# Optimization experiments

Measured on AMD Instinct MI355X. Metric: run time of the kernel, lower is better.

Reference implementation:

```python
import jax, jax.numpy as jnp
import numpy as np

B, S, D, H = 4, 2048, 1024, 16
HD = D // H  # head dim = 64

def setup_inputs() -> dict:
    key = jax.random.key(0)
    ks = jax.random.split(key, 11)
    s = 1.0 / np.sqrt(D)
    return {
        "q": jax.random.normal(ks[0], (B, S, D), jnp.float32),
        "k": jax.random.normal(ks[1], (B, S, D), jnp.float32),
        "v": jax.random.normal(ks[2], (B, S, D), jnp.float32),
        "Wq": jax.random.normal(ks[3], (D, D), jnp.float32) * s,
        "bq": jnp.zeros((D,), jnp.float32),
        "Wk": jax.random.normal(ks[4], (D, D), jnp.float32) * s,
        "bk": jnp.zeros((D,), jnp.float32),
        "Wv": jax.random.normal(ks[5], (D, D), jnp.float32) * s,
        "bv": jnp.zeros((D,), jnp.float32),
        "Wo": jax.random.normal(ks[6], (D, D), jnp.float32) * s,
        "bo": jnp.zeros((D,), jnp.float32),
    }

def reference(q, k, v, Wq, bq, Wk, bk, Wv, bv, Wo, bo):
    b, n, _ = q.shape
    # QKV projections, split heads -> [b, s, h, hd]
    qh = (q @ Wq + bq).reshape(b, n, H, HD)
    kh = (k @ Wk + bk).reshape(b, k.shape[1], H, HD)
    vh = (v @ Wv + bv).reshape(b, v.shape[1], H, HD)
    scale = 1.0 / np.sqrt(HD)
    scores = jnp.einsum('blhe,bshe->bhls', qh, kh)  # [b,h,l,s]
    attn = jax.nn.softmax(scale * scores, axis=-1)  # dropout is identity in eval
    out = jnp.einsum('bhls,bshd->blhd', attn, vh)   # [b,l,h,hd]
    out = out.reshape(b, n, H * HD)
    return out @ Wo + bo
```

## Files before the change

### kernel.cpp

```cpp
#include <hip/hip_runtime.h>
#include <cstdint>

#define DEV __device__ __forceinline__

typedef __attribute__((ext_vector_type(8))) __bf16 bf16x8;
typedef __attribute__((ext_vector_type(2))) unsigned u32x2;
typedef __attribute__((ext_vector_type(4))) float f32x4;

DEV unsigned short f2b(float f) {
  unsigned u = __builtin_bit_cast(unsigned, f);
  u += 0x7fffu + ((u >> 16) & 1u);
  return (unsigned short)(u >> 16);
}

DEV unsigned pkrn(float f0, float f1) {
  unsigned a0 = __builtin_bit_cast(unsigned, f0) + 0x8000u;
  unsigned a1 = __builtin_bit_cast(unsigned, f1) + 0x8000u;
#if __has_builtin(__builtin_amdgcn_perm)
  return __builtin_amdgcn_perm(a1, a0, 0x07060302u);
#else
  return (a0 >> 16) | (a1 & 0xffff0000u);
#endif
}

DEV float exp2_fast(float x) {
#if __has_builtin(__builtin_amdgcn_exp2f)
  return __builtin_amdgcn_exp2f(x);
#else
  return __expf(x * 0.6931471805599453f);
#endif
}

DEV void gload_lds16(const unsigned short* g, unsigned short* l) {
  __builtin_amdgcn_global_load_lds(
      (const __attribute__((address_space(1))) void*)g,
      (__attribute__((address_space(3))) void*)l, 16, 0, 0);
}

__global__ __launch_bounds__(256) void cvt3_kernel(const float* __restrict__ q,
                                                   const float* __restrict__ k,
                                                   const float* __restrict__ v,
                                                   unsigned short* __restrict__ dst) {
  int z = blockIdx.y;
  const float* src = (z == 0) ? q : (z == 1) ? k : v;
  unsigned short* d = dst + (size_t)z * 8192 * 1024;
  int i = blockIdx.x * 256 + threadIdx.x;
  const float4* s4 = (const float4*)src;
  float4 a = s4[2 * i], b = s4[2 * i + 1];
  uint4 o;
  o.x = (unsigned)f2b(a.x) | ((unsigned)f2b(a.y) << 16);
  o.y = (unsigned)f2b(a.z) | ((unsigned)f2b(a.w) << 16);
  o.z = (unsigned)f2b(b.x) | ((unsigned)f2b(b.y) << 16);
  o.w = (unsigned)f2b(b.z) | ((unsigned)f2b(b.w) << 16);
  ((uint4*)d)[i] = o;
}

__global__ __launch_bounds__(256) void wtr4_kernel(const float* __restrict__ W0,
                                                   const float* __restrict__ W1,
                                                   const float* __restrict__ W2,
                                                   const float* __restrict__ W3,
                                                   unsigned short* __restrict__ WtBase) {
  int z = blockIdx.z;
  const float* W = (z == 0) ? W0 : (z == 1) ? W1 : (z == 2) ? W2 : W3;
  unsigned short* Wt = WtBase + (size_t)z * 1024 * 1024;
  __shared__ float t[64][65];
  int n0 = blockIdx.x * 64, k0 = blockIdx.y * 64;
  int tx = threadIdx.x & 63, ty = threadIdx.x >> 6;
  for (int i = ty; i < 64; i += 4)
    t[i][tx] = W[(size_t)(k0 + i) * 1024 + n0 + tx];
  __syncthreads();
  for (int i = ty; i < 64; i += 4)
    Wt[(size_t)(n0 + i) * 1024 + k0 + tx] = f2b(t[tx][i]);
}

struct GemmAcc {
  f32x4 acc[4][4];
};

DEV void gemm_core(const unsigned short* __restrict__ A,
                   const unsigned short* __restrict__ Bt,
                   unsigned short* Al, unsigned short* Bl,
                   int m0, int n0, int K, GemmAcc& R) {
  int tid = threadIdx.x, wv = tid >> 6, ln = tid & 63;
  int wr = wv >> 1, wc = wv & 1;
  for (int i = 0; i < 4; i++)
    for (int j = 0; j < 4; j++) R.acc[i][j] = (f32x4)0.f;
  int lr = ln >> 3, lc = (ln & 7) * 8;
  for (int kt = 0; kt < K; kt += 64) {
    __syncthreads();
    for (int o = 0; o < 4; ++o) {
      int op = wv * 4 + o;
      int row = op * 8 + lr;
      gload_lds16(A + (size_t)(m0 + row) * K + kt + lc, &Al[op * 512]);
    }
    for (int o = 0; o < 4; ++o) {
      int op = wv * 4 + o;
      int row = op * 8 + lr;
      gload_lds16(Bt + (size_t)(n0 + row) * K + kt + lc, &Bl[op * 512]);
    }
    __syncthreads();
    for (int kk = 0; kk < 2; ++kk) {
      bf16x8 af[4], bfr[4];
      int ko = kk * 32 + (ln >> 4) * 8;
      for (int i = 0; i < 4; ++i)
        af[i] = *(const bf16x8*)&Al[(wr * 64 + i * 16 + (ln & 15)) * 64 + ko];
      for (int j = 0; j < 4; ++j)
        bfr[j] = *(const bf16x8*)&Bl[(wc * 64 + j * 16 + (ln & 15)) * 64 + ko];
      for (int i = 0; i < 4; ++i)
        for (int j = 0; j < 4; ++j)
          R.acc[i][j] = __builtin_amdgcn_mfma_f32_16x16x32_bf16(af[i], bfr[j], R.acc[i][j], 0, 0, 0);
    }
  }
}

__global__ __launch_bounds__(256) void gemm_qkv(const unsigned short* __restrict__ Xbase,
                                                const unsigned short* __restrict__ Wbase,
                                                const float* __restrict__ bq,
                                                const float* __restrict__ bk,
                                                const float* __restrict__ bv,
                                                unsigned short* __restrict__ Obase,
                                                float qscale) {
  __shared__ unsigned short Al[128 * 64];
  __shared__ unsigned short Bl[128 * 64];
  int z = blockIdx.z;
  const size_t NX = (size_t)8192 * 1024, NW = (size_t)1024 * 1024;
  const unsigned short* A = Xbase + (size_t)z * NX;
  const unsigned short* Bt = Wbase + (size_t)z * NW;
  const float* bias = (z == 0) ? bq : (z == 1) ? bk : bv;
  unsigned short* outp = Obase + (size_t)z * NX;
  int m0 = blockIdx.y * 128, n0 = blockIdx.x * 128;
  GemmAcc R;
  gemm_core(A, Bt, Al, Bl, m0, n0, 1024, R);
  int ln = threadIdx.x & 63, wv = threadIdx.x >> 6;
  int wr = wv >> 1, wc = wv & 1;
  int g = ln >> 4, c = ln & 15;
  if (z < 2) {
    float oscale = (z == 0) ? qscale : 1.0f;
    for (int j = 0; j < 4; ++j) {
      int gn = n0 + wc * 64 + j * 16 + c;
      float bs = bias[gn];
      int h_ = gn >> 6, hd = gn & 63;
      for (int i = 0; i < 4; ++i) {
        int gm0 = m0 + wr * 64 + i * 16 + g * 4;
        for (int r = 0; r < 4; ++r) {
          float vv = (R.acc[i][j][r] + bs) * oscale;
          int gm = gm0 + r;
          int b_ = gm >> 11, s_ = gm & 2047;
          outp[(((size_t)(b_ * 16 + h_) * 2048 + s_) << 6) + hd] = f2b(vv);
        }
      }
    }
  } else {
    int mb = m0 + wr * 64;
    int b_ = mb >> 11, st = (mb & 2047) >> 6;
    for (int j = 0; j < 4; ++j) {
      int gn = n0 + wc * 64 + j * 16 + c;
      float bs = bias[gn];
      int h_ = gn >> 6, hd = gn & 63;
      unsigned short* vrow = outp + (((size_t)((b_ * 16 + h_) * 32 + st) * 64 + hd) << 6);
      for (int r = 0; r < 4; ++r) {
        u32x2 w;
        w.x = pkrn(R.acc[0][j][r] + bs, R.acc[1][j][r] + bs);
        w.y = pkrn(R.acc[2][j][r] + bs, R.acc[3][j][r] + bs);
        *(u32x2*)&vrow[(g * 4 + r) * 4] = w;
      }
    }
  }
}

__global__ __launch_bounds__(256) void gemm_out(const unsigned short* __restrict__ A,
                                                const unsigned short* __restrict__ Bt,
                                                const float* __restrict__ bias,
                                                float* __restrict__ outp) {
  __shared__ unsigned short Al[128 * 64];
  __shared__ unsigned short Bl[128 * 64];
  int m0 = blockIdx.y * 128, n0 = blockIdx.x * 128;
  GemmAcc R;
  gemm_core(A, Bt, Al, Bl, m0, n0, 1024, R);
  int ln = threadIdx.x & 63, wv = threadIdx.x >> 6;
  int wr = wv >> 1, wc = wv & 1;
  int g = ln >> 4, c = ln & 15;
  for (int j = 0; j < 4; ++j) {
    int gn = n0 + wc * 64 + j * 16 + c;
    float bs = bias[gn];
    for (int i = 0; i < 4; ++i) {
      int gm0 = m0 + wr * 64 + i * 16 + g * 4;
      for (int r = 0; r < 4; ++r)
        outp[(size_t)(gm0 + r) * 1024 + gn] = R.acc[i][j][r] + bs;
    }
  }
}

__global__ __launch_bounds__(256) void attn_kernel(const unsigned short* __restrict__ Qh,
                                                   const unsigned short* __restrict__ Kh,
                                                   const unsigned short* __restrict__ VtG,
                                                   unsigned short* __restrict__ AttnOut) {
  __shared__ unsigned short Kl[64 * 64];
  __shared__ unsigned short Vl[64 * 64];
  __shared__ unsigned short Pl[4 * 32 * 72];
  int tid = threadIdx.x, wv = tid >> 6, ln = tid & 63;
  int qt = blockIdx.x, bh = blockIdx.y;
  const unsigned short* Qb = Qh + (size_t)bh * 2048 * 64;
  const unsigned short* Kb = Kh + (size_t)bh * 2048 * 64;
  const unsigned short* Vb = VtG + (size_t)bh * 2048 * 64;
  int q0 = qt * 128 + wv * 32;
  int g = ln >> 4, c = ln & 15;
  int lr = ln >> 3, lb = ln & 7;
  bf16x8 aq[2][2];
  for (int mi = 0; mi < 2; ++mi)
    for (int kk = 0; kk < 2; ++kk)
      aq[mi][kk] = *(const bf16x8*)(Qb + (size_t)(q0 + mi * 16 + c) * 64 + kk * 32 + g * 8);
  f32x4 o[2][4], lrun[2];
  for (int mi = 0; mi < 2; ++mi) {
    lrun[mi] = (f32x4)0.f;
    for (int j = 0; j < 4; ++j) o[mi][j] = (f32x4)0.f;
  }
  unsigned short* pw = &Pl[wv * 32 * 72];
  for (int kt = 0; kt < 2048; kt += 64) {
    __syncthreads();
    for (int ot = 0; ot < 2; ++ot) {
      int rb = wv * 16 + ot * 8;
      gload_lds16(Kb + (size_t)(kt + rb + lr) * 64 + (lb ^ lr) * 8, &Kl[rb * 64]);
    }
    const unsigned short* vtb = Vb + (size_t)(kt >> 6) * 4096;
    for (int ot = 0; ot < 2; ++ot) {
      int rb = wv * 16 + ot * 8;
      gload_lds16(vtb + (size_t)(rb + lr) * 64 + (lb ^ lr) * 8, &Vl[rb * 64]);
    }
    __syncthreads();
    f32x4 s[2][4];
    for (int mi = 0; mi < 2; ++mi)
      for (int j = 0; j < 4; ++j) s[mi][j] = (f32x4)0.f;
    for (int kk = 0; kk < 2; ++kk) {
      bf16x8 bk[4];
      for (int j = 0; j < 4; ++j)
        bk[j] = *(const bf16x8*)&Kl[(j * 16 + c) * 64 + ((kk * 4 + g) ^ (c & 7)) * 8];
      for (int mi = 0; mi < 2; ++mi)
        for (int j = 0; j < 4; ++j)
          s[mi][j] = __builtin_amdgcn_mfma_f32_16x16x32_bf16(aq[mi][kk], bk[j], s[mi][j], 0, 0, 0);
    }
    for (int mi = 0; mi < 2; ++mi)
      for (int j = 0; j < 4; ++j)
        for (int r = 0; r < 4; ++r) {
          float p = exp2_fast(s[mi][j][r]);
          s[mi][j][r] = p;
          lrun[mi][r] += p;
        }
    for (int mi = 0; mi < 2; ++mi)
      for (int r = 0; r < 4; ++r) {
        u32x2 w;
        w.x = pkrn(s[mi][0][r], s[mi][1][r]);
        w.y = pkrn(s[mi][2][r], s[mi][3][r]);
        *(u32x2*)&pw[(mi * 16 + g * 4 + r) * 72 + c * 4] = w;
      }
    __threadfence_block();
    for (int kk = 0; kk < 2; ++kk) {
      int ko = kk * 32 + g * 8;
      bf16x8 ap[2], bv[4];
      for (int mi = 0; mi < 2; ++mi) ap[mi] = *(const bf16x8*)&pw[(mi * 16 + c) * 72 + ko];
      for (int j = 0; j < 4; ++j)
        bv[j] = *(const bf16x8*)&Vl[(j * 16 + c) * 64 + ((kk * 4 + g) ^ (c & 7)) * 8];
      for (int mi = 0; mi < 2; ++mi)
        for (int j = 0; j < 4; ++j)
          o[mi][j] = __builtin_amdgcn_mfma_f32_16x16x32_bf16(ap[mi], bv[j], o[mi][j], 0, 0, 0);
    }
  }
  int b_ = bh >> 4, h_ = bh & 15;
  for (int mi = 0; mi < 2; ++mi) {
    float linv[4];
    for (int r = 0; r < 4; ++r) {
      float l = lrun[mi][r];
      for (int d = 1; d < 16; d <<= 1) l += __shfl_xor(l, d);
      linv[r] = 1.f / l;
    }
    for (int j = 0; j < 4; ++j)
      for (int r = 0; r < 4; ++r) {
        int row = q0 + mi * 16 + g * 4 + r;
        int col = h_ * 64 + j * 16 + c;
        float val = o[mi][j][r] * linv[r];
        AttnOut[((size_t)b_ * 2048 + row) * 1024 + col] = f2b(val);
      }
  }
}

extern "C" void kernel_launch(void* const* d_in, const int* in_sizes, int n_in,
                              void* d_out, int out_size, void* d_ws, size_t ws_size,
                              hipStream_t stream) {
  const float* q  = (const float*)d_in[0];
  const float* k  = (const float*)d_in[1];
  const float* v  = (const float*)d_in[2];
  const float* Wq = (const float*)d_in[3];
  const float* bq = (const float*)d_in[4];
  const float* Wk = (const float*)d_in[5];
  const float* bk = (const float*)d_in[6];
  const float* Wv = (const float*)d_in[7];
  const float* bv = (const float*)d_in[8];
  const float* Wo = (const float*)d_in[9];
  const float* bo = (const float*)d_in[10];
  float* out = (float*)d_out;

  unsigned short* ws = (unsigned short*)d_ws;
  const size_t NX = (size_t)8192 * 1024;
  const size_t NW = (size_t)1024 * 1024;
  unsigned short* X   = ws;
  unsigned short* Wt  = X + 3 * NX;
  unsigned short* QKV = Wt + 4 * NW;
  unsigned short* Ao  = X;

  const float qscale = 0.125f * 1.4426950408889634f;

  cvt3_kernel<<<dim3(4096, 3), 256, 0, stream>>>(q, k, v, X);
  wtr4_kernel<<<dim3(16, 16, 4), 256, 0, stream>>>(Wq, Wk, Wv, Wo, Wt);
  gemm_qkv<<<dim3(8, 64, 3), 256, 0, stream>>>(X, Wt, bq, bk, bv, QKV, qscale);
  attn_kernel<<<dim3(16, 64), 256, 0, stream>>>(QKV, QKV + NX, QKV + 2 * NX, Ao);
  gemm_out<<<dim3(8, 64), 256, 0, stream>>>(Ao, Wt + 3 * NW, bo, out);
}
```

Measured before the change: 373.7 us.

## Double-buffer LDS tiles in GEMM and attention loops to overlap loads

Both the shared GEMM core and the attention kernel now keep two LDS buffers for their operand tiles. The first tile is loaded before the loop, and each iteration issues the async global-to-LDS loads for the next tile before computing on the current one. This leaves one barrier per iteration instead of two, so memory latency can hide behind MFMA work. The cost is twice the LDS for those tiles (64 KB per GEMM block), which may lower how many blocks fit per CU.

```diff
diff --git a/kernel.cpp b/kernel.cpp
--- a/kernel.cpp
+++ b/kernel.cpp
@@ -86,26 +86,31 @@
   for (int i = 0; i < 4; i++)
     for (int j = 0; j < 4; j++) R.acc[i][j] = (f32x4)0.f;
   int lr = ln >> 3, lc = (ln & 7) * 8;
-  for (int kt = 0; kt < K; kt += 64) {
+  int nk = K >> 6;
+  for (int o = 0; o < 4; ++o) {
+    int op = wv * 4 + o, row = op * 8 + lr;
+    gload_lds16(A + (size_t)(m0 + row) * K + lc, &Al[op * 512]);
+    gload_lds16(Bt + (size_t)(n0 + row) * K + lc, &Bl[op * 512]);
+  }
+  for (int it = 0; it < nk; ++it) {
     __syncthreads();
-    for (int o = 0; o < 4; ++o) {
-      int op = wv * 4 + o;
-      int row = op * 8 + lr;
-      gload_lds16(A + (size_t)(m0 + row) * K + kt + lc, &Al[op * 512]);
-    }
-    for (int o = 0; o < 4; ++o) {
-      int op = wv * 4 + o;
-      int row = op * 8 + lr;
-      gload_lds16(Bt + (size_t)(n0 + row) * K + kt + lc, &Bl[op * 512]);
-    }
-    __syncthreads();
+    int cur = (it & 1) * 8192;
+    if (it + 1 < nk) {
+      int nxt = ((it + 1) & 1) * 8192;
+      int kt = (it + 1) << 6;
+      for (int o = 0; o < 4; ++o) {
+        int op = wv * 4 + o, row = op * 8 + lr;
+        gload_lds16(A + (size_t)(m0 + row) * K + kt + lc, &Al[nxt + op * 512]);
+        gload_lds16(Bt + (size_t)(n0 + row) * K + kt + lc, &Bl[nxt + op * 512]);
+      }
+    }
     for (int kk = 0; kk < 2; ++kk) {
       bf16x8 af[4], bfr[4];
       int ko = kk * 32 + (ln >> 4) * 8;
       for (int i = 0; i < 4; ++i)
-        af[i] = *(const bf16x8*)&Al[(wr * 64 + i * 16 + (ln & 15)) * 64 + ko];
+        af[i] = *(const bf16x8*)&Al[cur + (wr * 64 + i * 16 + (ln & 15)) * 64 + ko];
       for (int j = 0; j < 4; ++j)
-        bfr[j] = *(const bf16x8*)&Bl[(wc * 64 + j * 16 + (ln & 15)) * 64 + ko];
+        bfr[j] = *(const bf16x8*)&Bl[cur + (wc * 64 + j * 16 + (ln & 15)) * 64 + ko];
       for (int i = 0; i < 4; ++i)
         for (int j = 0; j < 4; ++j)
           R.acc[i][j] = __builtin_amdgcn_mfma_f32_16x16x32_bf16(af[i], bfr[j], R.acc[i][j], 0, 0, 0);
@@ -120,8 +125,8 @@
                                                 const float* __restrict__ bv,
                                                 unsigned short* __restrict__ Obase,
                                                 float qscale) {
-  __shared__ unsigned short Al[128 * 64];
-  __shared__ unsigned short Bl[128 * 64];
+  __shared__ unsigned short Al[2 * 128 * 64];
+  __shared__ unsigned short Bl[2 * 128 * 64];
   int z = blockIdx.z;
   const size_t NX = (size_t)8192 * 1024, NW = (size_t)1024 * 1024;
   const unsigned short* A = Xbase + (size_t)z * NX;
@@ -172,8 +177,8 @@
                                                 const unsigned short* __restrict__ Bt,
                                                 const float* __restrict__ bias,
                                                 float* __restrict__ outp) {
-  __shared__ unsigned short Al[128 * 64];
-  __shared__ unsigned short Bl[128 * 64];
+  __shared__ unsigned short Al[2 * 128 * 64];
+  __shared__ unsigned short Bl[2 * 128 * 64];
   int m0 = blockIdx.y * 128, n0 = blockIdx.x * 128;
   GemmAcc R;
   gemm_core(A, Bt, Al, Bl, m0, n0, 1024, R);
@@ -195,8 +200,8 @@
                                                    const unsigned short* __restrict__ Kh,
                                                    const unsigned short* __restrict__ VtG,
                                                    unsigned short* __restrict__ AttnOut) {
-  __shared__ unsigned short Kl[64 * 64];
-  __shared__ unsigned short Vl[64 * 64];
+  __shared__ unsigned short Kl[2 * 64 * 64];
+  __shared__ unsigned short Vl[2 * 64 * 64];
   __shared__ unsigned short Pl[4 * 32 * 72];
   int tid = threadIdx.x, wv = tid >> 6, ln = tid & 63;
   int qt = blockIdx.x, bh = blockIdx.y;
@@ -206,6 +211,7 @@
   int q0 = qt * 128 + wv * 32;
   int g = ln >> 4, c = ln & 15;
   int lr = ln >> 3, lb = ln & 7;
+  int swz = (lb ^ lr) * 8;
   bf16x8 aq[2][2];
   for (int mi = 0; mi < 2; ++mi)
     for (int kk = 0; kk < 2; ++kk)
@@ -216,25 +222,31 @@
     for (int j = 0; j < 4; ++j) o[mi][j] = (f32x4)0.f;
   }
   unsigned short* pw = &Pl[wv * 32 * 72];
-  for (int kt = 0; kt < 2048; kt += 64) {
+  for (int ot = 0; ot < 2; ++ot) {
+    int rb = wv * 16 + ot * 8;
+    gload_lds16(Kb + (size_t)(rb + lr) * 64 + swz, &Kl[rb * 64]);
+    gload_lds16(Vb + (size_t)(rb + lr) * 64 + swz, &Vl[rb * 64]);
+  }
+  for (int t = 0; t < 32; ++t) {
     __syncthreads();
-    for (int ot = 0; ot < 2; ++ot) {
-      int rb = wv * 16 + ot * 8;
-      gload_lds16(Kb + (size_t)(kt + rb + lr) * 64 + (lb ^ lr) * 8, &Kl[rb * 64]);
-    }
-    const unsigned short* vtb = Vb + (size_t)(kt >> 6) * 4096;
-    for (int ot = 0; ot < 2; ++ot) {
-      int rb = wv * 16 + ot * 8;
-      gload_lds16(vtb + (size_t)(rb + lr) * 64 + (lb ^ lr) * 8, &Vl[rb * 64]);
-    }
-    __syncthreads();
+    int cur = (t & 1) * 4096;
+    if (t + 1 < 32) {
+      int nxt = ((t + 1) & 1) * 4096;
+      const unsigned short* kb = Kb + (size_t)(t + 1) * 4096;
+      const unsigned short* vb = Vb + (size_t)(t + 1) * 4096;
+      for (int ot = 0; ot < 2; ++ot) {
+        int rb = wv * 16 + ot * 8;
+        gload_lds16(kb + (size_t)(rb + lr) * 64 + swz, &Kl[nxt + rb * 64]);
+        gload_lds16(vb + (size_t)(rb + lr) * 64 + swz, &Vl[nxt + rb * 64]);
+      }
+    }
     f32x4 s[2][4];
     for (int mi = 0; mi < 2; ++mi)
       for (int j = 0; j < 4; ++j) s[mi][j] = (f32x4)0.f;
     for (int kk = 0; kk < 2; ++kk) {
       bf16x8 bk[4];
       for (int j = 0; j < 4; ++j)
-        bk[j] = *(const bf16x8*)&Kl[(j * 16 + c) * 64 + ((kk * 4 + g) ^ (c & 7)) * 8];
+        bk[j] = *(const bf16x8*)&Kl[cur + (j * 16 + c) * 64 + ((kk * 4 + g) ^ (c & 7)) * 8];
       for (int mi = 0; mi < 2; ++mi)
         for (int j = 0; j < 4; ++j)
           s[mi][j] = __builtin_amdgcn_mfma_f32_16x16x32_bf16(aq[mi][kk], bk[j], s[mi][j], 0, 0, 0);
@@ -259,7 +271,7 @@
       bf16x8 ap[2], bv[4];
       for (int mi = 0; mi < 2; ++mi) ap[mi] = *(const bf16x8*)&pw[(mi * 16 + c) * 72 + ko];
       for (int j = 0; j < 4; ++j)
-        bv[j] = *(const bf16x8*)&Vl[(j * 16 + c) * 64 + ((kk * 4 + g) ^ (c & 7)) * 8];
+        bv[j] = *(const bf16x8*)&Vl[cur + (j * 16 + c) * 64 + ((kk * 4 + g) ^ (c & 7)) * 8];
       for (int mi = 0; mi < 2; ++mi)
         for (int j = 0; j < 4; ++j)
           o[mi][j] = __builtin_amdgcn_mfma_f32_16x16x32_bf16(ap[mi], bv[j], o[mi][j], 0, 0, 0);
```

Result: slower. 384.0 us (+2.8%).

## Double-buffer K/V tiles in attention, switch P and V to fp16, sum rows via MFMA

Applied to the files above, without the earlier changes.

The attention loop now double-buffers K and V in LDS, prefetching the next tile with global_load_lds while the current one is computed, and needs only one barrier per iteration instead of two. Softmax probabilities and V are packed as fp16 with cvt_pkrtz and multiplied with f16 MFMA. Row sums are taken by an extra MFMA against a ones vector, replacing the scalar accumulation and the cross-lane shuffle reduction. The GEMM epilogues also precompute store base addresses. Using fp16 for V and P changes precision and range, and relies on the Q/K projection code producing V in fp16.

```diff
diff --git a/kernel.cpp b/kernel.cpp
--- a/kernel.cpp
+++ b/kernel.cpp
@@ -4,6 +4,8 @@
 #define DEV __device__ __forceinline__
 
 typedef __attribute__((ext_vector_type(8))) __bf16 bf16x8;
+typedef __attribute__((ext_vector_type(8))) _Float16 f16x8;
+typedef __attribute__((ext_vector_type(2))) __fp16 fp16x2;
 typedef __attribute__((ext_vector_type(2))) unsigned u32x2;
 typedef __attribute__((ext_vector_type(4))) float f32x4;
 
@@ -13,14 +15,9 @@
   return (unsigned short)(u >> 16);
 }
 
-DEV unsigned pkrn(float f0, float f1) {
-  unsigned a0 = __builtin_bit_cast(unsigned, f0) + 0x8000u;
-  unsigned a1 = __builtin_bit_cast(unsigned, f1) + 0x8000u;
-#if __has_builtin(__builtin_amdgcn_perm)
-  return __builtin_amdgcn_perm(a1, a0, 0x07060302u);
-#else
-  return (a0 >> 16) | (a1 & 0xffff0000u);
-#endif
+DEV unsigned pkhf(float a, float b) {
+  fp16x2 h = __builtin_amdgcn_cvt_pkrtz(a, b);
+  return __builtin_bit_cast(unsigned, h);
 }
 
 DEV float exp2_fast(float x) {
@@ -134,25 +131,21 @@
   int ln = threadIdx.x & 63, wv = threadIdx.x >> 6;
   int wr = wv >> 1, wc = wv & 1;
   int g = ln >> 4, c = ln & 15;
+  int mb = m0 + wr * 64;
+  int b_ = mb >> 11, sb = mb & 2047;
   if (z < 2) {
     float oscale = (z == 0) ? qscale : 1.0f;
     for (int j = 0; j < 4; ++j) {
       int gn = n0 + wc * 64 + j * 16 + c;
       float bs = bias[gn];
       int h_ = gn >> 6, hd = gn & 63;
-      for (int i = 0; i < 4; ++i) {
-        int gm0 = m0 + wr * 64 + i * 16 + g * 4;
-        for (int r = 0; r < 4; ++r) {
-          float vv = (R.acc[i][j][r] + bs) * oscale;
-          int gm = gm0 + r;
-          int b_ = gm >> 11, s_ = gm & 2047;
-          outp[(((size_t)(b_ * 16 + h_) * 2048 + s_) << 6) + hd] = f2b(vv);
-        }
-      }
+      unsigned short* base = outp + (((size_t)(b_ * 16 + h_) * 2048 + sb + g * 4) << 6) + hd;
+      for (int i = 0; i < 4; ++i)
+        for (int r = 0; r < 4; ++r)
+          base[i * 1024 + r * 64] = f2b((R.acc[i][j][r] + bs) * oscale);
     }
   } else {
-    int mb = m0 + wr * 64;
-    int b_ = mb >> 11, st = (mb & 2047) >> 6;
+    int st = sb >> 6;
     for (int j = 0; j < 4; ++j) {
       int gn = n0 + wc * 64 + j * 16 + c;
       float bs = bias[gn];
@@ -160,8 +153,8 @@
       unsigned short* vrow = outp + (((size_t)((b_ * 16 + h_) * 32 + st) * 64 + hd) << 6);
       for (int r = 0; r < 4; ++r) {
         u32x2 w;
-        w.x = pkrn(R.acc[0][j][r] + bs, R.acc[1][j][r] + bs);
-        w.y = pkrn(R.acc[2][j][r] + bs, R.acc[3][j][r] + bs);
+        w.x = pkhf(R.acc[0][j][r] + bs, R.acc[1][j][r] + bs);
+        w.y = pkhf(R.acc[2][j][r] + bs, R.acc[3][j][r] + bs);
         *(u32x2*)&vrow[(g * 4 + r) * 4] = w;
       }
     }
@@ -183,11 +176,10 @@
   for (int j = 0; j < 4; ++j) {
     int gn = n0 + wc * 64 + j * 16 + c;
     float bs = bias[gn];
-    for (int i = 0; i < 4; ++i) {
-      int gm0 = m0 + wr * 64 + i * 16 + g * 4;
+    float* base = outp + (size_t)(m0 + wr * 64 + g * 4) * 1024 + gn;
+    for (int i = 0; i < 4; ++i)
       for (int r = 0; r < 4; ++r)
-        outp[(size_t)(gm0 + r) * 1024 + gn] = R.acc[i][j][r] + bs;
-    }
+        base[(i * 16 + r) * 1024] = R.acc[i][j][r] + bs;
   }
 }
 
@@ -195,8 +187,8 @@
                                                    const unsigned short* __restrict__ Kh,
                                                    const unsigned short* __restrict__ VtG,
                                                    unsigned short* __restrict__ AttnOut) {
-  __shared__ unsigned short Kl[64 * 64];
-  __shared__ unsigned short Vl[64 * 64];
+  __shared__ unsigned short Kl[2 * 64 * 64];
+  __shared__ unsigned short Vl[2 * 64 * 64];
   __shared__ unsigned short Pl[4 * 32 * 72];
   int tid = threadIdx.x, wv = tid >> 6, ln = tid & 63;
   int qt = blockIdx.x, bh = blockIdx.y;
@@ -206,73 +198,84 @@
   int q0 = qt * 128 + wv * 32;
   int g = ln >> 4, c = ln & 15;
   int lr = ln >> 3, lb = ln & 7;
+  int swz = (lb ^ lr) * 8;
   bf16x8 aq[2][2];
   for (int mi = 0; mi < 2; ++mi)
     for (int kk = 0; kk < 2; ++kk)
       aq[mi][kk] = *(const bf16x8*)(Qb + (size_t)(q0 + mi * 16 + c) * 64 + kk * 32 + g * 8);
-  f32x4 o[2][4], lrun[2];
+  f32x4 o[2][4], ladd[2];
   for (int mi = 0; mi < 2; ++mi) {
-    lrun[mi] = (f32x4)0.f;
+    ladd[mi] = (f32x4)0.f;
     for (int j = 0; j < 4; ++j) o[mi][j] = (f32x4)0.f;
   }
+  const f32x4 z4 = {0.f, 0.f, 0.f, 0.f};
+  f16x8 ones;
+  for (int i = 0; i < 8; ++i) ones[i] = (_Float16)1.0f;
   unsigned short* pw = &Pl[wv * 32 * 72];
-  for (int kt = 0; kt < 2048; kt += 64) {
+  int boff[2][4];
+  for (int kk = 0; kk < 2; ++kk)
+    for (int j = 0; j < 4; ++j) boff[kk][j] = (j * 16 + c) * 64 + (((kk * 4 + g) ^ (c & 7)) * 8);
+  int aoff[2][2];
+  for (int mi = 0; mi < 2; ++mi)
+    for (int kk = 0; kk < 2; ++kk) aoff[mi][kk] = (mi * 16 + c) * 72 + kk * 32 + g * 8;
+  int poff[2][4];
+  for (int mi = 0; mi < 2; ++mi)
+    for (int r = 0; r < 4; ++r) poff[mi][r] = (mi * 16 + g * 4 + r) * 72 + c * 4;
+  int rb0 = wv * 16, rb1 = wv * 16 + 8;
+  gload_lds16(Kb + (size_t)(rb0 + lr) * 64 + swz, &Kl[rb0 * 64]);
+  gload_lds16(Kb + (size_t)(rb1 + lr) * 64 + swz, &Kl[rb1 * 64]);
+  gload_lds16(Vb + (size_t)(rb0 + lr) * 64 + swz, &Vl[rb0 * 64]);
+  gload_lds16(Vb + (size_t)(rb1 + lr) * 64 + swz, &Vl[rb1 * 64]);
+  const unsigned short* kg0 = Kb + 4096 + (size_t)(rb0 + lr) * 64 + swz;
+  const unsigned short* kg1 = Kb + 4096 + (size_t)(rb1 + lr) * 64 + swz;
+  const unsigned short* vg0 = Vb + 4096 + (size_t)(rb0 + lr) * 64 + swz;
+  const unsigned short* vg1 = Vb + 4096 + (size_t)(rb1 + lr) * 64 + swz;
+  for (int t = 0; t < 32; ++t) {
     __syncthreads();
-    for (int ot = 0; ot < 2; ++ot) {
-      int rb = wv * 16 + ot * 8;
-      gload_lds16(Kb + (size_t)(kt + rb + lr) * 64 + (lb ^ lr) * 8, &Kl[rb * 64]);
-    }
-    const unsigned short* vtb = Vb + (size_t)(kt >> 6) * 4096;
-    for (int ot = 0; ot < 2; ++ot) {
-      int rb = wv * 16 + ot * 8;
-      gload_lds16(vtb + (size_t)(rb + lr) * 64 + (lb ^ lr) * 8, &Vl[rb * 64]);
-    }
-    __syncthreads();
+    int cur = (t & 1) * 4096;
+    if (t + 1 < 32) {
+      int nxt = cur ^ 4096;
+      gload_lds16(kg0, &Kl[nxt + rb0 * 64]);
+      gload_lds16(kg1, &Kl[nxt + rb1 * 64]);
+      gload_lds16(vg0, &Vl[nxt + rb0 * 64]);
+      gload_lds16(vg1, &Vl[nxt + rb1 * 64]);
+      kg0 += 4096; kg1 += 4096; vg0 += 4096; vg1 += 4096;
+    }
     f32x4 s[2][4];
-    for (int mi = 0; mi < 2; ++mi)
-      for (int j = 0; j < 4; ++j) s[mi][j] = (f32x4)0.f;
-    for (int kk = 0; kk < 2; ++kk) {
+    {
       bf16x8 bk[4];
-      for (int j = 0; j < 4; ++j)
-        bk[j] = *(const bf16x8*)&Kl[(j * 16 + c) * 64 + ((kk * 4 + g) ^ (c & 7)) * 8];
+      for (int j = 0; j < 4; ++j) bk[j] = *(const bf16x8*)&Kl[cur + boff[0][j]];
       for (int mi = 0; mi < 2; ++mi)
         for (int j = 0; j < 4; ++j)
-          s[mi][j] = __builtin_amdgcn_mfma_f32_16x16x32_bf16(aq[mi][kk], bk[j], s[mi][j], 0, 0, 0);
-    }
-    for (int mi = 0; mi < 2; ++mi)
-      for (int j = 0; j < 4; ++j)
-        for (int r = 0; r < 4; ++r) {
-          float p = exp2_fast(s[mi][j][r]);
-          s[mi][j][r] = p;
-          lrun[mi][r] += p;
-        }
+          s[mi][j] = __builtin_amdgcn_mfma_f32_16x16x32_bf16(aq[mi][0], bk[j], z4, 0, 0, 0);
+      for (int j = 0; j < 4; ++j) bk[j] = *(const bf16x8*)&Kl[cur + boff[1][j]];
+      for (int mi = 0; mi < 2; ++mi)
+        for (int j = 0; j < 4; ++j)
+          s[mi][j] = __builtin_amdgcn_mfma_f32_16x16x32_bf16(aq[mi][1], bk[j], s[mi][j], 0, 0, 0);
+    }
     for (int mi = 0; mi < 2; ++mi)
       for (int r = 0; r < 4; ++r) {
         u32x2 w;
-        w.x = pkrn(s[mi][0][r], s[mi][1][r]);
-        w.y = pkrn(s[mi][2][r], s[mi][3][r]);
-        *(u32x2*)&pw[(mi * 16 + g * 4 + r) * 72 + c * 4] = w;
+        w.x = pkhf(exp2_fast(s[mi][0][r]), exp2_fast(s[mi][1][r]));
+        w.y = pkhf(exp2_fast(s[mi][2][r]), exp2_fast(s[mi][3][r]));
+        *(u32x2*)&pw[poff[mi][r]] = w;
       }
     __threadfence_block();
     for (int kk = 0; kk < 2; ++kk) {
-      int ko = kk * 32 + g * 8;
-      bf16x8 ap[2], bv[4];
-      for (int mi = 0; mi < 2; ++mi) ap[mi] = *(const bf16x8*)&pw[(mi * 16 + c) * 72 + ko];
-      for (int j = 0; j < 4; ++j)
-        bv[j] = *(const bf16x8*)&Vl[(j * 16 + c) * 64 + ((kk * 4 + g) ^ (c & 7)) * 8];
+      f16x8 ap[2], bv[4];
+      for (int mi = 0; mi < 2; ++mi) ap[mi] = *(const f16x8*)&pw[aoff[mi][kk]];
+      for (int j = 0; j < 4; ++j) bv[j] = *(const f16x8*)&Vl[cur + boff[kk][j]];
+      for (int mi = 0; mi < 2; ++mi)
+        ladd[mi] = __builtin_amdgcn_mfma_f32_16x16x32_f16(ap[mi], ones, ladd[mi], 0, 0, 0);
       for (int mi = 0; mi < 2; ++mi)
         for (int j = 0; j < 4; ++j)
-          o[mi][j] = __builtin_amdgcn_mfma_f32_16x16x32_bf16(ap[mi], bv[j], o[mi][j], 0, 0, 0);
+          o[mi][j] = __builtin_amdgcn_mfma_f32_16x16x32_f16(ap[mi], bv[j], o[mi][j], 0, 0, 0);
     }
   }
   int b_ = bh >> 4, h_ = bh & 15;
   for (int mi = 0; mi < 2; ++mi) {
     float linv[4];
-    for (int r = 0; r < 4; ++r) {
-      float l = lrun[mi][r];
-      for (int d = 1; d < 16; d <<= 1) l += __shfl_xor(l, d);
-      linv[r] = 1.f / l;
-    }
+    for (int r = 0; r < 4; ++r) linv[r] = 1.f / ladd[mi][r];
     for (int j = 0; j < 4; ++j)
       for (int r = 0; r < 4; ++r) {
         int row = q0 + mi * 16 + g * 4 + r;
```

After: 389.2 us. 1.04x slower.
